# Performance work log

Hardware: AMD Instinct MI355X
Metric: run time of the kernel (lower is better)

## Reference

```python
import jax, jax.numpy as jnp
import numpy as np

DT = 0.01
REG = 0.01

def setup_inputs() -> dict:
    key = jax.random.key(0)
    k1, k2, k3, k4 = jax.random.split(key, 4)
    B, C_in, L = 16, 128, 4096
    C_out, KS = 256, 9
    return {
        "x": jax.random.normal(k1, (B, C_in, L), dtype=jnp.float32),
        "weight": jax.random.normal(k2, (C_out, C_in, KS), dtype=jnp.float32) * np.sqrt(2.0 / (C_out * KS)),
        "bias": jnp.zeros((C_out,), dtype=jnp.float32),
        "vel": jax.random.normal(k3, (C_in, KS), dtype=jnp.float32) * 0.1,
        "acc": jax.random.normal(k4, (C_in, KS), dtype=jnp.float32) * 0.01,
        "ks": 9,
        "stride": 1,
        "pad": 4,
    }

def reference(x, weight, bias, vel, acc, ks, stride, pad):
    # x: [B, C_in, L]
    if pad > 0:
        x = jnp.pad(x, ((0, 0), (0, 0), (pad, pad)), mode="edge")  # replicate pad
    L_pad = x.shape[2]
    L_out = (L_pad - ks) // stride + 1
    t_off = jnp.arange(ks, dtype=jnp.float32) * DT  # [ks]
    # unfold: gather sliding windows -> [B, C_in, L_out, ks]
    idx = jnp.arange(L_out)[:, None] * stride + jnp.arange(ks)[None, :]
    xu = x[:, :, idx]
    # per-tap physics offset: vel*t + 0.5*acc*t^2, shape [C_in, ks] broadcast
    offset = vel * t_off + 0.5 * acc * (t_off ** 2)  # [C_in, ks]
    xt = xu + offset[None, :, None, :]  # [B, C_in, L_out, ks]
    # GEMM: [B, L_out, C_in*ks] x [C_in*ks, C_out]
    out = jnp.einsum("bclk,ock->bol", xt, weight) + bias[None, :, None]
    phys = REG * (jnp.mean(vel ** 2) + jnp.mean(acc ** 2))
    return (out, phys)
```

## Files before the change

### kernel.cpp

```cpp
#include <hip/hip_runtime.h>
#include <hip/hip_bf16.h>

typedef unsigned short u16;
typedef __bf16 bf16x8 __attribute__((ext_vector_type(8)));
typedef float f32x4 __attribute__((ext_vector_type(4)));
typedef float f32x16 __attribute__((ext_vector_type(16)));
typedef unsigned short ushort8 __attribute__((ext_vector_type(8)));

#define C_IN   128
#define C_OUT  256
#define BATCH  16
#define LEN    4096
#define KS     9
#define PAD    4
#define KTOT   (C_IN * KS)
#define NSTEP  72

#define W5_BLKS    1152
#define EB_BLKS    256

__device__ inline u16 f2bf(float f) {
    __hip_bfloat16 h = __float2bfloat16(f);
    return __builtin_bit_cast(u16, h);
}

__global__ void prep_all(const float* __restrict__ w,
                         const float* __restrict__ bias, const float* __restrict__ vel,
                         const float* __restrict__ acc_in,
                         u16* __restrict__ w5,
                         float* __restrict__ ebias, float* __restrict__ phys_out) {
    int bid = blockIdx.x;
    int t = threadIdx.x;
    if (bid < W5_BLKS) {
        int i = bid * 256 + t;
        int e    = i & 7;
        int lane = (i >> 3) & 63;
        int g    = (i >> 9) & 7;
        int s    = i >> 12;
        int o    = g * 32 + (lane & 31);
        int hi   = lane >> 5;
        int c    = (s & 7) * 16 + hi * 8 + e;
        int k    = s >> 3;
        w5[i] = f2bf(w[((size_t)o * C_IN + c) * KS + k]);
        return;
    }
    __shared__ float red[256];
    int o = bid - W5_BLKS;
    float sum = 0.f;
    for (int i = t; i < KTOT; i += 256) {
        int k = i % KS;
        float tk = k * 0.01f;
        float off = vel[i] * tk + 0.5f * acc_in[i] * tk * tk;
        sum += off * w[(size_t)o * KTOT + i];
    }
    red[t] = sum;
    __syncthreads();
    for (int h = 128; h > 0; h >>= 1) {
        if (t < h) red[t] += red[t + h];
        __syncthreads();
    }
    if (t == 0) ebias[o] = bias[o] + red[0];

    if (o == 0) {
        __syncthreads();
        float pv = 0.f;
        for (int i = t; i < KTOT; i += 256) {
            float v = vel[i], a = acc_in[i];
            pv += v * v + a * a;
        }
        red[t] = pv;
        __syncthreads();
        for (int h = 128; h > 0; h >>= 1) {
            if (t < h) red[t] += red[t + h];
            __syncthreads();
        }
        if (t == 0) *phys_out = 0.01f * (red[0] / (float)KTOT);
    }
}

__global__ __launch_bounds__(128, 1) void conv_main(const float* __restrict__ x,
                                                    const u16* __restrict__ w5,
                                                    const float* __restrict__ ebias,
                                                    float* __restrict__ out) {
    __shared__ u16 ldsx[17408];

    int b     = blockIdx.y;
    int lbase = blockIdx.x * 128;
    int t     = threadIdx.x;
    int lane  = t & 63;
    int wm    = t >> 6;
    int l31   = lane & 31;
    int hi    = lane >> 5;

    const u16* alane = w5 + ((size_t)(wm * 4) * 64 + lane) * 8;

    #define LOAD_A(S, AF)                                                        \
        {                                                                        \
            const u16* p_ = alane + (size_t)(S) * 4096;                          \
            _Pragma("unroll")                                                    \
            for (int mi = 0; mi < 4; ++mi)                                       \
                AF[mi] = *reinterpret_cast<const bf16x8*>(p_ + mi * 512);        \
        }
    #define LOAD_B(S, BF)                                                        \
        {                                                                        \
            int k_ = (S) >> 3;                                                   \
            int sl_ = ((S) & 7) * 2 + hi;                                        \
            _Pragma("unroll")                                                    \
            for (int nj = 0; nj < 4; ++nj) {                                     \
                int row_  = nj * 32 + l31 + k_;                                  \
                int addr_ = row_ * 256 + ((sl_ ^ (row_ & 15)) << 4);             \
                BF[nj] = *reinterpret_cast<const bf16x8*>(ldsbase + addr_);      \
            }                                                                    \
        }
    #define MFMA16(AF, BF)                                                       \
        {                                                                        \
            _Pragma("unroll")                                                    \
            for (int mi = 0; mi < 4; ++mi)                                       \
                _Pragma("unroll")                                                \
                for (int nj = 0; nj < 4; ++nj)                                   \
                    acc[mi][nj] = __builtin_amdgcn_mfma_f32_32x32x16_bf16(       \
                        AF[mi], BF[nj], acc[mi][nj], 0, 0, 0);                   \
        }

    bf16x8 aA[4], aB[4], bA[4], bB[4];
    LOAD_A(0, aA);

    const float* xb = x + (size_t)b * C_IN * LEN;
    {
        int r = t;
        int l = lbase + r - PAD;
        l = l < 0 ? 0 : (l > LEN - 1 ? LEN - 1 : l);
        int key = r & 15;
        float v[16][8];
        #pragma unroll
        for (int cb = 0; cb < 16; ++cb)
            #pragma unroll
            for (int e = 0; e < 8; ++e)
                v[cb][e] = xb[(size_t)(cb * 8 + e) * LEN + l];
        #pragma unroll
        for (int cb = 0; cb < 16; ++cb) {
            ushort8 u;
            #pragma unroll
            for (int e = 0; e < 8; ++e) u[e] = f2bf(v[cb][e]);
            *reinterpret_cast<ushort8*>(ldsx + r * 128 + ((cb ^ key) * 8)) = u;
        }
    }
    {
        int r  = 128 + (t & 7);
        int cb = t >> 3;
        int l = lbase + r - PAD;
        l = l < 0 ? 0 : (l > LEN - 1 ? LEN - 1 : l);
        ushort8 u;
        #pragma unroll
        for (int e = 0; e < 8; ++e)
            u[e] = f2bf(xb[(size_t)(cb * 8 + e) * LEN + l]);
        *reinterpret_cast<ushort8*>(ldsx + r * 128 + ((cb ^ (r & 15)) * 8)) = u;
    }
    __syncthreads();

    f32x16 acc[4][4] = {};
    const char* ldsbase = reinterpret_cast<const char*>(ldsx);
    LOAD_B(0, bA);

    #pragma unroll
    for (int s = 0; s < NSTEP; s += 2) {
        LOAD_A(s + 1, aB);
        LOAD_B(s + 1, bB);
        MFMA16(aA, bA);
        if (s + 2 < NSTEP) { LOAD_A(s + 2, aA); LOAD_B(s + 2, bA); }
        MFMA16(aB, bB);
    }

    #pragma unroll
    for (int mi = 0; mi < 4; ++mi) {
        int o0 = wm * 128 + mi * 32 + hi * 4;
        #pragma unroll
        for (int nj = 0; nj < 4; ++nj) {
            int l = lbase + nj * 32 + l31;
            #pragma unroll
            for (int q = 0; q < 4; ++q) {
                f32x4 eb = *reinterpret_cast<const f32x4*>(ebias + o0 + q * 8);
                float* op = out + (size_t)(b * C_OUT + o0 + q * 8) * LEN + l;
                #pragma unroll
                for (int p = 0; p < 4; ++p)
                    op[(size_t)p * LEN] = acc[mi][nj][q * 4 + p] + eb[p];
            }
        }
    }
    #undef LOAD_A
    #undef LOAD_B
    #undef MFMA16
}

extern "C" void kernel_launch(void* const* d_in, const int* in_sizes, int n_in,
                              void* d_out, int out_size, void* d_ws, size_t ws_size,
                              hipStream_t stream) {
    const float* x      = (const float*)d_in[0];
    const float* weight = (const float*)d_in[1];
    const float* bias   = (const float*)d_in[2];
    const float* vel    = (const float*)d_in[3];
    const float* acc    = (const float*)d_in[4];
    float* out = (float*)d_out;

    char* ws = (char*)d_ws;
    u16*  w5    = (u16*)ws;
    float* ebias = (float*)(ws + (size_t)C_OUT * KTOT * 2);

    hipLaunchKernelGGL(prep_all, dim3(W5_BLKS + EB_BLKS), dim3(256), 0, stream,
                       weight, bias, vel, acc, w5, ebias,
                       out + (size_t)BATCH * C_OUT * LEN);
    hipLaunchKernelGGL(conv_main, dim3(LEN / 128, BATCH), dim3(128), 0, stream,
                       x, w5, ebias, out);
}
```

Measured before the change: 52.11 us.

## Split output tile into two sequential passes with triple-buffered operand prefetch

```diff
diff --git a/kernel.cpp b/kernel.cpp
--- a/kernel.cpp
+++ b/kernel.cpp
@@ -92,39 +92,6 @@
     int l31   = lane & 31;
     int hi    = lane >> 5;
 
-    const u16* alane = w5 + ((size_t)(wm * 4) * 64 + lane) * 8;
-
-    #define LOAD_A(S, AF)                                                        \
-        {                                                                        \
-            const u16* p_ = alane + (size_t)(S) * 4096;                          \
-            _Pragma("unroll")                                                    \
-            for (int mi = 0; mi < 4; ++mi)                                       \
-                AF[mi] = *reinterpret_cast<const bf16x8*>(p_ + mi * 512);        \
-        }
-    #define LOAD_B(S, BF)                                                        \
-        {                                                                        \
-            int k_ = (S) >> 3;                                                   \
-            int sl_ = ((S) & 7) * 2 + hi;                                        \
-            _Pragma("unroll")                                                    \
-            for (int nj = 0; nj < 4; ++nj) {                                     \
-                int row_  = nj * 32 + l31 + k_;                                  \
-                int addr_ = row_ * 256 + ((sl_ ^ (row_ & 15)) << 4);             \
-                BF[nj] = *reinterpret_cast<const bf16x8*>(ldsbase + addr_);      \
-            }                                                                    \
-        }
-    #define MFMA16(AF, BF)                                                       \
-        {                                                                        \
-            _Pragma("unroll")                                                    \
-            for (int mi = 0; mi < 4; ++mi)                                       \
-                _Pragma("unroll")                                                \
-                for (int nj = 0; nj < 4; ++nj)                                   \
-                    acc[mi][nj] = __builtin_amdgcn_mfma_f32_32x32x16_bf16(       \
-                        AF[mi], BF[nj], acc[mi][nj], 0, 0, 0);                   \
-        }
-
-    bf16x8 aA[4], aB[4], bA[4], bB[4];
-    LOAD_A(0, aA);
-
     const float* xb = x + (size_t)b * C_IN * LEN;
     {
         int r = t;
@@ -158,38 +125,75 @@
     }
     __syncthreads();
 
-    f32x16 acc[4][4] = {};
     const char* ldsbase = reinterpret_cast<const char*>(ldsx);
-    LOAD_B(0, bA);
-
-    #pragma unroll
-    for (int s = 0; s < NSTEP; s += 2) {
-        LOAD_A(s + 1, aB);
-        LOAD_B(s + 1, bB);
-        MFMA16(aA, bA);
-        if (s + 2 < NSTEP) { LOAD_A(s + 2, aA); LOAD_B(s + 2, bA); }
-        MFMA16(aB, bB);
-    }
-
-    #pragma unroll
-    for (int mi = 0; mi < 4; ++mi) {
-        int o0 = wm * 128 + mi * 32 + hi * 4;
-        #pragma unroll
-        for (int nj = 0; nj < 4; ++nj) {
-            int l = lbase + nj * 32 + l31;
-            #pragma unroll
-            for (int q = 0; q < 4; ++q) {
-                f32x4 eb = *reinterpret_cast<const f32x4*>(ebias + o0 + q * 8);
-                float* op = out + (size_t)(b * C_OUT + o0 + q * 8) * LEN + l;
-                #pragma unroll
-                for (int p = 0; p < 4; ++p)
-                    op[(size_t)p * LEN] = acc[mi][nj][q * 4 + p] + eb[p];
-            }
-        }
-    }
-    #undef LOAD_A
+
+    #define LOAD_A2(AP, S, AF)                                                   \
+        {                                                                        \
+            const u16* p_ = (AP) + (size_t)(S) * 4096;                           \
+            AF[0] = *reinterpret_cast<const bf16x8*>(p_);                        \
+            AF[1] = *reinterpret_cast<const bf16x8*>(p_ + 512);                  \
+        }
+    #define LOAD_B(S, BF)                                                        \
+        {                                                                        \
+            int k_ = (S) >> 3;                                                   \
+            int sl_ = ((S) & 7) * 2 + hi;                                        \
+            _Pragma("unroll")                                                    \
+            for (int nj = 0; nj < 4; ++nj) {                                     \
+                int row_  = nj * 32 + l31 + k_;                                  \
+                int addr_ = row_ * 256 + ((sl_ ^ (row_ & 15)) << 4);             \
+                BF[nj] = *reinterpret_cast<const bf16x8*>(ldsbase + addr_);      \
+            }                                                                    \
+        }
+    #define MFMA8(AF, BF)                                                        \
+        {                                                                        \
+            _Pragma("unroll")                                                    \
+            for (int mi = 0; mi < 2; ++mi)                                       \
+                _Pragma("unroll")                                                \
+                for (int nj = 0; nj < 4; ++nj)                                   \
+                    acc[mi][nj] = __builtin_amdgcn_mfma_f32_32x32x16_bf16(       \
+                        AF[mi], BF[nj], acc[mi][nj], 0, 0, 0);                   \
+        }
+    #define RUN_PASS(P)                                                          \
+        {                                                                        \
+            const u16* ap_ = w5 + ((size_t)(wm * 4 + (P) * 2) * 64 + lane) * 8;  \
+            f32x16 acc[2][4] = {};                                               \
+            bf16x8 aA[2], aB[2], aC[2], bA[4], bB[4], bC[4];                     \
+            LOAD_A2(ap_, 0, aA); LOAD_B(0, bA);                                  \
+            LOAD_A2(ap_, 1, aB); LOAD_B(1, bB);                                  \
+            _Pragma("unroll")                                                    \
+            for (int s = 0; s < NSTEP; s += 3) {            \
+                if (s + 2 < NSTEP) { LOAD_A2(ap_, s + 2, aC); LOAD_B(s + 2, bC); } \
+                MFMA8(aA, bA);                                                   \
+                if (s + 3 < NSTEP) { LOAD_A2(ap_, s + 3, aA); LOAD_B(s + 3, bA); } \
+                MFMA8(aB, bB);                                                   \
+                if (s + 4 < NSTEP) { LOAD_A2(ap_, s + 4, aB); LOAD_B(s + 4, bB); } \
+                if (s + 2 < NSTEP) MFMA8(aC, bC);                                \
+            }                                                                    \
+            _Pragma("unroll")                                                    \
+            for (int mi = 0; mi < 2; ++mi) {                                     \
+                int o0 = wm * 128 + ((P) * 2 + mi) * 32 + hi * 4;                \
+                _Pragma("unroll")                                                \
+                for (int nj = 0; nj < 4; ++nj) {                                 \
+                    int l = lbase + nj * 32 + l31;                               \
+                    _Pragma("unroll")                                            \
+                    for (int q = 0; q < 4; ++q) {                                \
+                        f32x4 eb = *reinterpret_cast<const f32x4*>(ebias + o0 + q * 8); \
+                        float* op = out + (size_t)(b * C_OUT + o0 + q * 8) * LEN + l;   \
+                        _Pragma("unroll")                                        \
+                        for (int p2 = 0; p2 < 4; ++p2)                           \
+                            op[(size_t)p2 * LEN] = acc[mi][nj][q * 4 + p2] + eb[p2];    \
+                    }                                                            \
+                }                                                                \
+            }                                                                    \
+        }
+
+    RUN_PASS(0);
+    RUN_PASS(1);
+
+    #undef LOAD_A2
     #undef LOAD_B
-    #undef MFMA16
+    #undef MFMA8
+    #undef RUN_PASS
 }
 
 extern "C" void kernel_launch(void* const* d_in, const int* in_sizes, int n_in,
```

Measured after the change: 97.19 us. 86.5% more time.
